# Optimization experiments

Measured on AMD Instinct MI355X. Metric: run time of the kernel, lower is better.

## Reference

```python
import jax, jax.numpy as jnp
import numpy as np

N = 50000      # nodes
E = 800000     # edges (before self-loops)
F_IN = 128     # num_features
H = 4          # heads
C = 64         # hidden_channels
HC = H * C     # 256
NEG_SLOPE = 0.2


def setup_inputs() -> dict:
    key = jax.random.key(0)
    ks = jax.random.split(key, 20)
    x = jax.random.normal(ks[0], (N, F_IN), dtype=jnp.float32)
    edge_index = jax.random.randint(ks[1], (2, E), 0, N, dtype=jnp.int32)
    s = 0.05
    inp = {"x": x, "edge_index": edge_index}
    dims_in = [F_IN, HC, HC, HC]
    for l in range(4):
        kW, ka, kb = jax.random.split(ks[2 + l], 3)
        inp[f"W{l+1}"] = jax.random.normal(kW, (dims_in[l], HC), dtype=jnp.float32) * s
        inp[f"a_src{l+1}"] = jax.random.normal(ka, (H, C), dtype=jnp.float32) * s
        inp[f"a_dst{l+1}"] = jax.random.normal(kb, (H, C), dtype=jnp.float32) * s
        inp[f"b{l+1}"] = jnp.zeros((HC,), dtype=jnp.float32)
    return inp


def gat_conv(x, src, dst, W, a_src, a_dst, b):
    # x: [N, F_in] -> h: [N, H, C]
    h = (x @ W).reshape(N, H, C)
    es = jnp.sum(h * a_src, axis=-1)  # [N, H] per-node source logits
    ed = jnp.sum(h * a_dst, axis=-1)  # [N, H]
    e = jax.nn.leaky_relu(es[src] + ed[dst], NEG_SLOPE)  # [Etot, H]
    m = jax.ops.segment_max(e, dst, num_segments=N)      # per-dst max
    m = jnp.where(jnp.isfinite(m), m, 0.0)
    ex = jnp.exp(e - m[dst])
    denom = jax.ops.segment_sum(ex, dst, num_segments=N)
    alpha = ex / (denom[dst] + 1e-16)                     # edge softmax
    out = jax.ops.segment_sum(alpha[:, :, None] * h[src], dst, num_segments=N)
    return out.reshape(N, HC) + b


def reference(x, edge_index,
              W1, a_src1, a_dst1, b1,
              W2, a_src2, a_dst2, b2,
              W3, a_src3, a_dst3, b3,
              W4, a_src4, a_dst4, b4):
    loop = jnp.arange(N, dtype=edge_index.dtype)
    src = jnp.concatenate([edge_index[0], loop])  # add self-loops (PyG default)
    dst = jnp.concatenate([edge_index[1], loop])
    x1 = jax.nn.relu(gat_conv(x, src, dst, W1, a_src1, a_dst1, b1))
    x2 = jax.nn.relu(gat_conv(x1, src, dst, W2, a_src2, a_dst2, b2))
    x3 = jax.nn.relu(gat_conv(x2 + x1, src, dst, W3, a_src3, a_dst3, b3))
    x4 = jax.nn.relu(gat_conv(x2 + x3, src, dst, W4, a_src4, a_dst4, b4))
    # NOTE: source code calls conv4 again (not conv5) -- reproduced faithfully
    x5 = gat_conv(x4 + x3, src, dst, W4, a_src4, a_dst4, b4)
    return x5
```

## Files before the change

### kernel.cpp

```cpp
#include <hip/hip_runtime.h>
#include <hip/hip_bf16.h>

#define N_NODES 50000
#define E_EDGES 800000
#define ETOT (E_EDGES + N_NODES)
#define HC 256
#define NHEAD 4
#define CHAN 64
#define NEG 0.2f
#define NBLK ((N_NODES + 1023) / 1024)

typedef _Float16 half8 __attribute__((ext_vector_type(8)));
typedef _Float16 half4v __attribute__((ext_vector_type(4)));
typedef float float4v __attribute__((ext_vector_type(4)));


__global__ void count_kernel(const int* __restrict__ ei, int* __restrict__ counts) {
    int i = blockIdx.x * blockDim.x + threadIdx.x;
    if (i >= ETOT) return;
    int dst = (i < E_EDGES) ? ei[E_EDGES + i] : (i - E_EDGES);
    atomicAdd(&counts[dst], 1);
}

__global__ __launch_bounds__(256) void blocksum_kernel(const int* __restrict__ counts,
                                                       int* __restrict__ blocksums) {
    __shared__ int s[4];
    int b = blockIdx.x, tid = threadIdx.x;
    int base = b * 1024;
    int sum = 0;
    #pragma unroll
    for (int r = 0; r < 4; ++r) {
        int idx = base + r * 256 + tid;
        sum += (idx < N_NODES) ? counts[idx] : 0;
    }
    #pragma unroll
    for (int m = 1; m < 64; m <<= 1) sum += __shfl_xor(sum, m, 64);
    if ((tid & 63) == 0) s[tid >> 6] = sum;
    __syncthreads();
    if (tid == 0) blocksums[b] = s[0] + s[1] + s[2] + s[3];
}

__global__ __launch_bounds__(64) void blockscan_kernel(int* __restrict__ blocksums) {
    int tid = threadIdx.x;
    int v = (tid < NBLK) ? blocksums[tid] : 0;
    #pragma unroll
    for (int off = 1; off < 64; off <<= 1) {
        int t = __shfl_up(v, off, 64);
        if (tid >= off) v += t;
    }
    if (tid < NBLK) blocksums[tid] = v;
}

__global__ __launch_bounds__(1024) void scatter_scan_kernel(const int* __restrict__ counts,
                                                            const int* __restrict__ blocksums,
                                                            int* __restrict__ offsets,
                                                            int* __restrict__ cursor) {
    __shared__ int s[1024];
    int b = blockIdx.x, tid = threadIdx.x;
    int idx = b * 1024 + tid;
    int v = (idx < N_NODES) ? counts[idx] : 0;
    s[tid] = v;
    __syncthreads();
    for (int off = 1; off < 1024; off <<= 1) {
        int t = (tid >= off) ? s[tid - off] : 0;
        __syncthreads();
        s[tid] += t;
        __syncthreads();
    }
    int excl = s[tid] - v + (b > 0 ? blocksums[b - 1] : 0);
    if (idx < N_NODES) { offsets[idx] = excl; cursor[idx] = excl; }
    if (idx == N_NODES - 1) offsets[N_NODES] = excl + v;
}

__global__ void fill_kernel(const int* __restrict__ ei, int* __restrict__ cursor,
                            int* __restrict__ csr_src) {
    int i = blockIdx.x * blockDim.x + threadIdx.x;
    if (i >= ETOT) return;
    int src, dst;
    if (i < E_EDGES) { src = ei[i]; dst = ei[E_EDGES + i]; }
    else             { src = i - E_EDGES; dst = src; }
    int pos = atomicAdd(&cursor[dst], 1);
    csr_src[pos] = src;
}


__global__ void wsplit_kernel(const float* __restrict__ W, _Float16* __restrict__ Wth,
                              _Float16* __restrict__ Wtl, int K) {
    int id = blockIdx.x * 256 + threadIdx.x;
    if (id >= K * 256) return;
    int n = id & 255, k = id >> 8;
    float w = W[(size_t)k * 256 + n];
    _Float16 h = (_Float16)w;
    _Float16 l = (_Float16)(w - (float)h);
    Wth[(size_t)n * K + k] = h;
    Wtl[(size_t)n * K + k] = l;
}

__global__ void xsplit_kernel(const float* __restrict__ x, _Float16* __restrict__ xh,
                              _Float16* __restrict__ xl, int total) {
    int id = blockIdx.x * 256 + threadIdx.x;
    if (id >= total) return;
    float v = x[id];
    _Float16 h = (_Float16)v;
    xh[id] = h;
    xl[id] = (_Float16)(v - (float)h);
}


#define LDK 40

__global__ __launch_bounds__(256) void gemm_mfma_kernel(
        const _Float16* __restrict__ A1h, const _Float16* __restrict__ A1l,
        const _Float16* __restrict__ A2h,
        const _Float16* __restrict__ Wth, const _Float16* __restrict__ Wtl,
        const float* __restrict__ a_src, const float* __restrict__ a_dst,
        _Float16* __restrict__ H16, float* __restrict__ es, float* __restrict__ ed,
        int M, int K) {
    __shared__ _Float16 Ah[64][LDK];
    __shared__ _Float16 Al[64][LDK];
    __shared__ _Float16 Bh[256][LDK];
    __shared__ _Float16 Bl[256][LDK];

    int tid = threadIdx.x;
    int m0 = blockIdx.x * 64;
    int w = tid >> 6, lane = tid & 63;
    int rn = w * 64;
    int fr = lane & 15;
    int q  = lane >> 4;
    int fk = q * 8;

    int wr = tid >> 2;
    int wk = (tid & 3) * 8;

    bool has_lo = (A1l != nullptr);
    bool has2   = (A2h != nullptr);

    float4v acc[4][4];
    #pragma unroll
    for (int i = 0; i < 4; ++i)
        #pragma unroll
        for (int j = 0; j < 4; ++j)
            acc[i][j] = (float4v){0.f, 0.f, 0.f, 0.f};

    half8 pa, pal, pbh[4], pbl[4];

    auto load_tile = [&](int k0) {
        int row = m0 + wr;
        pa  = (half8)(_Float16)0;
        pal = (half8)(_Float16)0;
        if (row < M) {
            pa = *(const half8*)(A1h + (size_t)row * K + k0 + wk);
            if (has2) {
                half8 u = *(const half8*)(A2h + (size_t)row * K + k0 + wk);
                pa = pa + u;
            }
            if (has_lo) pal = *(const half8*)(A1l + (size_t)row * K + k0 + wk);
        }
        #pragma unroll
        for (int g = 0; g < 4; ++g) {
            int r = g * 64 + wr;
            pbh[g] = *(const half8*)(Wth + (size_t)r * K + k0 + wk);
            pbl[g] = *(const half8*)(Wtl + (size_t)r * K + k0 + wk);
        }
    };

    load_tile(0);
    for (int k0 = 0; k0 < K; k0 += 32) {
        *(half8*)&Ah[wr][wk] = pa;
        if (has_lo) *(half8*)&Al[wr][wk] = pal;
        #pragma unroll
        for (int g = 0; g < 4; ++g) {
            int r = g * 64 + wr;
            *(half8*)&Bh[r][wk] = pbh[g];
            *(half8*)&Bl[r][wk] = pbl[g];
        }
        __syncthreads();
        if (k0 + 32 < K) load_tile(k0 + 32);
        half8 afh[4], bfh[4], bfl[4];
        #pragma unroll
        for (int t = 0; t < 4; ++t) {
            afh[t] = *(const half8*)&Ah[t * 16 + fr][fk];
            bfh[t] = *(const half8*)&Bh[rn + t * 16 + fr][fk];
            bfl[t] = *(const half8*)&Bl[rn + t * 16 + fr][fk];
        }
        if (has_lo) {
            half8 afl[4];
            #pragma unroll
            for (int t = 0; t < 4; ++t) afl[t] = *(const half8*)&Al[t * 16 + fr][fk];
            #pragma unroll
            for (int tm = 0; tm < 4; ++tm)
                #pragma unroll
                for (int tn = 0; tn < 4; ++tn)
                    acc[tm][tn] = __builtin_amdgcn_mfma_f32_16x16x32_f16(
                        afl[tm], bfh[tn], acc[tm][tn], 0, 0, 0);
        }
        #pragma unroll
        for (int tm = 0; tm < 4; ++tm)
            #pragma unroll
            for (int tn = 0; tn < 4; ++tn) {
                float4v c = acc[tm][tn];
                c = __builtin_amdgcn_mfma_f32_16x16x32_f16(afh[tm], bfl[tn], c, 0, 0, 0);
                c = __builtin_amdgcn_mfma_f32_16x16x32_f16(afh[tm], bfh[tn], c, 0, 0, 0);
                acc[tm][tn] = c;
            }
        __syncthreads();
    }

    float asv[4], adv[4];
    #pragma unroll
    for (int tn = 0; tn < 4; ++tn) {
        asv[tn] = a_src[w * CHAN + tn * 16 + fr];
        adv[tn] = a_dst[w * CHAN + tn * 16 + fr];
    }
    #pragma unroll
    for (int tm = 0; tm < 4; ++tm) {
        #pragma unroll
        for (int i = 0; i < 4; ++i) {
            int row = m0 + tm * 16 + q * 4 + i;
            float ps = 0.f, pd = 0.f;
            #pragma unroll
            for (int tn = 0; tn < 4; ++tn) {
                float hv = acc[tm][tn][i];
                ps += hv * asv[tn];
                pd += hv * adv[tn];
                if (row < M)
                    H16[(size_t)row * HC + rn + tn * 16 + fr] = (_Float16)hv;
            }
            #pragma unroll
            for (int msk = 1; msk < 16; msk <<= 1) {
                ps += __shfl_xor(ps, msk, 64);
                pd += __shfl_xor(pd, msk, 64);
            }
            if (fr == 0 && row < M) {
                es[row * NHEAD + w] = ps;
                ed[row * NHEAD + w] = pd;
            }
        }
    }
}


__global__ __launch_bounds__(256) void gat_aggregate_kernel(
        const _Float16* __restrict__ H16, const float* __restrict__ es, const float* __restrict__ ed,
        const int* __restrict__ offsets, const int* __restrict__ csr_src,
        const float* __restrict__ bias, _Float16* __restrict__ out16,
        float* __restrict__ out32, int do_relu) {
    __shared__ float ex_lds[4][256];
    __shared__ int   src_lds[4][64];
    int tid = threadIdx.x;
    int w = tid >> 6, lane = tid & 63;
    int n = blockIdx.x * 4 + w;
    int off = offsets[n];
    int deg = offsets[n + 1] - off;
    float4 edv = *(const float4*)(ed + (size_t)n * 4);

    if (deg <= 64) {
        int sreg = n;
        float4 ex4 = make_float4(0.f, 0.f, 0.f, 0.f);
        if (lane < deg) {
            sreg = csr_src[off + lane];
            float4 esv = *(const float4*)(es + (size_t)sreg * 4);
            float4 e4;
            e4.x = esv.x + edv.x; e4.y = esv.y + edv.y;
            e4.z = esv.z + edv.z; e4.w = esv.w + edv.w;
            e4.x = (e4.x > 0.f) ? e4.x : NEG * e4.x;
            e4.y = (e4.y > 0.f) ? e4.y : NEG * e4.y;
            e4.z = (e4.z > 0.f) ? e4.z : NEG * e4.z;
            e4.w = (e4.w > 0.f) ? e4.w : NEG * e4.w;
            ex4.x = __expf(e4.x); ex4.y = __expf(e4.y);
            ex4.z = __expf(e4.z); ex4.w = __expf(e4.w);
        }
        src_lds[w][lane] = sreg;
        *(float4*)&ex_lds[w][lane * 4] = ex4;

        int hl = lane & 31, side = lane >> 5;
        int hd = hl >> 3;
        float av[8] = {0.f, 0.f, 0.f, 0.f, 0.f, 0.f, 0.f, 0.f};
        int degr = (deg + 7) & ~7;
        #pragma unroll 2
        for (int j0 = 0; j0 < degr; j0 += 8) {
            int j = j0 + side;
            int s0 = src_lds[w][j];
            int s1 = src_lds[w][j + 2];
            int s2 = src_lds[w][j + 4];
            int s3 = src_lds[w][j + 6];
            float w0 = ex_lds[w][j * 4 + hd];
            float w1 = ex_lds[w][(j + 2) * 4 + hd];
            float w2 = ex_lds[w][(j + 4) * 4 + hd];
            float w3 = ex_lds[w][(j + 6) * 4 + hd];
            half8 h0 = *(const half8*)(H16 + (size_t)s0 * HC + hl * 8);
            half8 h1 = *(const half8*)(H16 + (size_t)s1 * HC + hl * 8);
            half8 h2 = *(const half8*)(H16 + (size_t)s2 * HC + hl * 8);
            half8 h3 = *(const half8*)(H16 + (size_t)s3 * HC + hl * 8);
            #pragma unroll
            for (int c = 0; c < 8; ++c) {
                av[c] += w0 * (float)h0[c];
                av[c] += w1 * (float)h1[c];
                av[c] += w2 * (float)h2[c];
                av[c] += w3 * (float)h3[c];
            }
        }

        float4 l4 = ex4;
        #pragma unroll
        for (int msk = 1; msk < 64; msk <<= 1) {
            l4.x += __shfl_xor(l4.x, msk, 64);
            l4.y += __shfl_xor(l4.y, msk, 64);
            l4.z += __shfl_xor(l4.z, msk, 64);
            l4.w += __shfl_xor(l4.w, msk, 64);
        }
        #pragma unroll
        for (int c = 0; c < 8; ++c) av[c] += __shfl_xor(av[c], 32, 64);
        if (side == 0) {
            float denom = (hd == 0) ? l4.x : (hd == 1) ? l4.y : (hd == 2) ? l4.z : l4.w;
            float scale = 1.f / (denom + 1e-16f);
            float4 b0 = *(const float4*)(bias + hl * 8);
            float4 b1 = *(const float4*)(bias + hl * 8 + 4);
            float o[8] = {av[0] * scale + b0.x, av[1] * scale + b0.y,
                          av[2] * scale + b0.z, av[3] * scale + b0.w,
                          av[4] * scale + b1.x, av[5] * scale + b1.y,
                          av[6] * scale + b1.z, av[7] * scale + b1.w};
            if (do_relu)
                #pragma unroll
                for (int c = 0; c < 8; ++c) o[c] = fmaxf(o[c], 0.f);
            if (out16) {
                half8 ov = {(_Float16)o[0], (_Float16)o[1], (_Float16)o[2], (_Float16)o[3],
                            (_Float16)o[4], (_Float16)o[5], (_Float16)o[6], (_Float16)o[7]};
                *(half8*)(out16 + (size_t)n * HC + hl * 8) = ov;
            } else {
                *(float4*)(out32 + (size_t)n * HC + hl * 8) =
                    make_float4(o[0], o[1], o[2], o[3]);
                *(float4*)(out32 + (size_t)n * HC + hl * 8 + 4) =
                    make_float4(o[4], o[5], o[6], o[7]);
            }
        }
        return;
    }

    int head = lane >> 4;
    float4 acc0 = make_float4(0.f, 0.f, 0.f, 0.f);
    float m[4] = {-1e30f, -1e30f, -1e30f, -1e30f};
    float l[4] = {0.f, 0.f, 0.f, 0.f};
    for (int base = 0; base < deg; base += 64) {
        int j = base + lane;
        if (j < deg) {
            int s = csr_src[off + j];
            float4 esv = *(const float4*)(es + (size_t)s * 4);
            float e[4] = {esv.x + edv.x, esv.y + edv.y, esv.z + edv.z, esv.w + edv.w};
            #pragma unroll
            for (int h = 0; h < 4; ++h) {
                e[h] = (e[h] > 0.f) ? e[h] : NEG * e[h];
                float M2 = fmaxf(m[h], e[h]);
                l[h] = l[h] * __expf(m[h] - M2) + __expf(e[h] - M2);
                m[h] = M2;
            }
        }
    }
    #pragma unroll
    for (int msk = 1; msk < 64; msk <<= 1) {
        #pragma unroll
        for (int h = 0; h < 4; ++h) {
            float mo = __shfl_xor(m[h], msk, 64);
            float lo = __shfl_xor(l[h], msk, 64);
            float M2 = fmaxf(m[h], mo);
            l[h] = l[h] * __expf(m[h] - M2) + lo * __expf(mo - M2);
            m[h] = M2;
        }
    }
    float fm = m[head];
    float fr2 = 1.f / (l[head] + 1e-16f);
    float edh = ((const float*)&edv)[head];
    for (int j = 0; j < deg; ++j) {
        int s = csr_src[off + j];
        float e = es[(size_t)s * 4 + head] + edh;
        e = (e > 0.f) ? e : NEG * e;
        float alpha = __expf(e - fm) * fr2;
        half4v h0 = *(const half4v*)(H16 + (size_t)s * HC + lane * 4);
        acc0.x += alpha * (float)h0[0]; acc0.y += alpha * (float)h0[1];
        acc0.z += alpha * (float)h0[2]; acc0.w += alpha * (float)h0[3];
    }
    float4 b4 = *(const float4*)(bias + lane * 4);
    float o[4] = {acc0.x + b4.x, acc0.y + b4.y, acc0.z + b4.z, acc0.w + b4.w};
    if (do_relu)
        #pragma unroll
        for (int c = 0; c < 4; ++c) o[c] = fmaxf(o[c], 0.f);
    if (out16) {
        half4v ov = {(_Float16)o[0], (_Float16)o[1], (_Float16)o[2], (_Float16)o[3]};
        *(half4v*)(out16 + (size_t)n * HC + lane * 4) = ov;
    } else {
        *(float4*)(out32 + (size_t)n * HC + lane * 4) = make_float4(o[0], o[1], o[2], o[3]);
    }
}


extern "C" void kernel_launch(void* const* d_in, const int* in_sizes, int n_in,
                              void* d_out, int out_size, void* d_ws, size_t ws_size,
                              hipStream_t stream) {
    const float* x  = (const float*)d_in[0];
    const int*   ei = (const int*)d_in[1];
    const float *W[5], *Asrc[5], *Adst[5], *Bs[5];
    for (int l = 0; l < 4; ++l) {
        W[l]    = (const float*)d_in[2 + l * 4];
        Asrc[l] = (const float*)d_in[3 + l * 4];
        Adst[l] = (const float*)d_in[4 + l * 4];
        Bs[l]   = (const float*)d_in[5 + l * 4];
    }
    W[4] = W[3]; Asrc[4] = Asrc[3]; Adst[4] = Adst[3]; Bs[4] = Bs[3];

    char* ws = (char*)d_ws;
    size_t off = 0;
    auto alloc = [&](size_t bytes) -> void* {
        void* p = ws + off;
        off += (bytes + 255) & ~(size_t)255;
        return p;
    };
    _Float16* h16  = (_Float16*)alloc((size_t)N_NODES * HC * 2);
    _Float16* xa   = (_Float16*)alloc((size_t)N_NODES * HC * 2);
    _Float16* xb   = (_Float16*)alloc((size_t)N_NODES * HC * 2);
    _Float16* xc   = (_Float16*)alloc((size_t)N_NODES * HC * 2);
    _Float16* xd   = (_Float16*)alloc((size_t)N_NODES * HC * 2);
    _Float16* xh   = (_Float16*)alloc((size_t)N_NODES * 128 * 2);
    _Float16* xl   = (_Float16*)alloc((size_t)N_NODES * 128 * 2);
    float* es      = (float*)alloc((size_t)N_NODES * 4 * 4);
    float* ed      = (float*)alloc((size_t)N_NODES * 4 * 4);
    int*   counts  = (int*)alloc((size_t)N_NODES * 4);
    int*   offsets = (int*)alloc((size_t)(N_NODES + 1) * 4);
    int*   cursor  = (int*)alloc((size_t)N_NODES * 4);
    int*   csr_src = (int*)alloc((size_t)ETOT * 4);
    int*   blocksums = (int*)alloc((size_t)NBLK * 4);
    _Float16 *Wth[5], *Wtl[5];
    int Ks[4] = {128, 256, 256, 256};
    for (int l = 0; l < 4; ++l) {
        Wth[l] = (_Float16*)alloc((size_t)256 * Ks[l] * 2);
        Wtl[l] = (_Float16*)alloc((size_t)256 * Ks[l] * 2);
    }
    Wth[4] = Wth[3]; Wtl[4] = Wtl[3];

    hipMemsetAsync(counts, 0, (size_t)N_NODES * 4, stream);
    count_kernel<<<(ETOT + 255) / 256, 256, 0, stream>>>(ei, counts);
    blocksum_kernel<<<NBLK, 256, 0, stream>>>(counts, blocksums);
    blockscan_kernel<<<1, 64, 0, stream>>>(blocksums);
    scatter_scan_kernel<<<NBLK, 1024, 0, stream>>>(counts, blocksums, offsets, cursor);
    fill_kernel<<<(ETOT + 255) / 256, 256, 0, stream>>>(ei, cursor, csr_src);
    for (int l = 0; l < 4; ++l)
        wsplit_kernel<<<(Ks[l] * 256 + 255) / 256, 256, 0, stream>>>(W[l], Wth[l], Wtl[l], Ks[l]);
    xsplit_kernel<<<(N_NODES * 128 + 255) / 256, 256, 0, stream>>>(x, xh, xl, N_NODES * 128);

    auto layer = [&](const _Float16* a1h, const _Float16* a1l, const _Float16* a2h,
                     int K, int l, _Float16* o16, float* o32, int relu) {
        gemm_mfma_kernel<<<(N_NODES + 63) / 64, 256, 0, stream>>>(
            a1h, a1l, a2h, Wth[l], Wtl[l], Asrc[l], Adst[l], h16, es, ed, N_NODES, K);
        gat_aggregate_kernel<<<N_NODES / 4, 256, 0, stream>>>(
            h16, es, ed, offsets, csr_src, Bs[l], o16, o32, relu);
    };

    float* out = (float*)d_out;
    layer(xh, xl,      nullptr, 128, 0, xa, nullptr, 1);
    layer(xa, nullptr, nullptr, 256, 1, xb, nullptr, 1);
    layer(xb, nullptr, xa,      256, 2, xc, nullptr, 1);
    layer(xb, nullptr, xc,      256, 3, xd, nullptr, 1);
    layer(xd, nullptr, xc,      256, 4, nullptr, out, 0);
}
```

Before: 792.2 us.

## Precompute per-edge attention exponentials in separate edge-parallel kernel

```diff
diff --git a/kernel.cpp b/kernel.cpp
--- a/kernel.cpp
+++ b/kernel.cpp
@@ -73,7 +73,7 @@
 }
 
 __global__ void fill_kernel(const int* __restrict__ ei, int* __restrict__ cursor,
-                            int* __restrict__ csr_src) {
+                            int* __restrict__ csr_src, int* __restrict__ csr_dst) {
     int i = blockIdx.x * blockDim.x + threadIdx.x;
     if (i >= ETOT) return;
     int src, dst;
@@ -81,6 +81,7 @@
     else             { src = i - E_EDGES; dst = src; }
     int pos = atomicAdd(&cursor[dst], 1);
     csr_src[pos] = src;
+    csr_dst[pos] = dst;
 }
 
 
@@ -104,6 +105,28 @@
     _Float16 h = (_Float16)v;
     xh[id] = h;
     xl[id] = (_Float16)(v - (float)h);
+}
+
+
+__global__ __launch_bounds__(256) void edge_alpha_kernel(
+        const float* __restrict__ es, const float* __restrict__ ed,
+        const int* __restrict__ csr_src, const int* __restrict__ csr_dst,
+        float* __restrict__ ex) {
+    int e = blockIdx.x * 256 + threadIdx.x;
+    if (e >= ETOT) return;
+    int s = csr_src[e], d = csr_dst[e];
+    float4 esv = *(const float4*)(es + (size_t)s * 4);
+    float4 edv = *(const float4*)(ed + (size_t)d * 4);
+    float4 v;
+    v.x = esv.x + edv.x; v.y = esv.y + edv.y;
+    v.z = esv.z + edv.z; v.w = esv.w + edv.w;
+    v.x = (v.x > 0.f) ? v.x : NEG * v.x;
+    v.y = (v.y > 0.f) ? v.y : NEG * v.y;
+    v.z = (v.z > 0.f) ? v.z : NEG * v.z;
+    v.w = (v.w > 0.f) ? v.w : NEG * v.w;
+    v.x = __expf(v.x); v.y = __expf(v.y);
+    v.z = __expf(v.z); v.w = __expf(v.w);
+    *(float4*)(ex + (size_t)e * 4) = v;
 }
 
 
@@ -241,7 +264,7 @@
 
 
 __global__ __launch_bounds__(256) void gat_aggregate_kernel(
-        const _Float16* __restrict__ H16, const float* __restrict__ es, const float* __restrict__ ed,
+        const _Float16* __restrict__ H16, const float* __restrict__ ex,
         const int* __restrict__ offsets, const int* __restrict__ csr_src,
         const float* __restrict__ bias, _Float16* __restrict__ out16,
         float* __restrict__ out32, int do_relu) {
@@ -252,23 +275,13 @@
     int n = blockIdx.x * 4 + w;
     int off = offsets[n];
     int deg = offsets[n + 1] - off;
-    float4 edv = *(const float4*)(ed + (size_t)n * 4);
 
     if (deg <= 64) {
         int sreg = n;
         float4 ex4 = make_float4(0.f, 0.f, 0.f, 0.f);
         if (lane < deg) {
             sreg = csr_src[off + lane];
-            float4 esv = *(const float4*)(es + (size_t)sreg * 4);
-            float4 e4;
-            e4.x = esv.x + edv.x; e4.y = esv.y + edv.y;
-            e4.z = esv.z + edv.z; e4.w = esv.w + edv.w;
-            e4.x = (e4.x > 0.f) ? e4.x : NEG * e4.x;
-            e4.y = (e4.y > 0.f) ? e4.y : NEG * e4.y;
-            e4.z = (e4.z > 0.f) ? e4.z : NEG * e4.z;
-            e4.w = (e4.w > 0.f) ? e4.w : NEG * e4.w;
-            ex4.x = __expf(e4.x); ex4.y = __expf(e4.y);
-            ex4.z = __expf(e4.z); ex4.w = __expf(e4.w);
+            ex4 = *(const float4*)(ex + (size_t)(off + lane) * 4);
         }
         src_lds[w][lane] = sreg;
         *(float4*)&ex_lds[w][lane * 4] = ex4;
@@ -339,48 +352,19 @@
 
     int head = lane >> 4;
     float4 acc0 = make_float4(0.f, 0.f, 0.f, 0.f);
-    float m[4] = {-1e30f, -1e30f, -1e30f, -1e30f};
-    float l[4] = {0.f, 0.f, 0.f, 0.f};
-    for (int base = 0; base < deg; base += 64) {
-        int j = base + lane;
-        if (j < deg) {
-            int s = csr_src[off + j];
-            float4 esv = *(const float4*)(es + (size_t)s * 4);
-            float e[4] = {esv.x + edv.x, esv.y + edv.y, esv.z + edv.z, esv.w + edv.w};
-            #pragma unroll
-            for (int h = 0; h < 4; ++h) {
-                e[h] = (e[h] > 0.f) ? e[h] : NEG * e[h];
-                float M2 = fmaxf(m[h], e[h]);
-                l[h] = l[h] * __expf(m[h] - M2) + __expf(e[h] - M2);
-                m[h] = M2;
-            }
-        }
-    }
-    #pragma unroll
-    for (int msk = 1; msk < 64; msk <<= 1) {
-        #pragma unroll
-        for (int h = 0; h < 4; ++h) {
-            float mo = __shfl_xor(m[h], msk, 64);
-            float lo = __shfl_xor(l[h], msk, 64);
-            float M2 = fmaxf(m[h], mo);
-            l[h] = l[h] * __expf(m[h] - M2) + lo * __expf(mo - M2);
-            m[h] = M2;
-        }
-    }
-    float fm = m[head];
-    float fr2 = 1.f / (l[head] + 1e-16f);
-    float edh = ((const float*)&edv)[head];
+    float den = 0.f;
     for (int j = 0; j < deg; ++j) {
         int s = csr_src[off + j];
-        float e = es[(size_t)s * 4 + head] + edh;
-        e = (e > 0.f) ? e : NEG * e;
-        float alpha = __expf(e - fm) * fr2;
+        float exv = ex[(size_t)(off + j) * 4 + head];
+        den += exv;
         half4v h0 = *(const half4v*)(H16 + (size_t)s * HC + lane * 4);
-        acc0.x += alpha * (float)h0[0]; acc0.y += alpha * (float)h0[1];
-        acc0.z += alpha * (float)h0[2]; acc0.w += alpha * (float)h0[3];
-    }
+        acc0.x += exv * (float)h0[0]; acc0.y += exv * (float)h0[1];
+        acc0.z += exv * (float)h0[2]; acc0.w += exv * (float)h0[3];
+    }
+    float scale = 1.f / (den + 1e-16f);
     float4 b4 = *(const float4*)(bias + lane * 4);
-    float o[4] = {acc0.x + b4.x, acc0.y + b4.y, acc0.z + b4.z, acc0.w + b4.w};
+    float o[4] = {acc0.x * scale + b4.x, acc0.y * scale + b4.y,
+                  acc0.z * scale + b4.z, acc0.w * scale + b4.w};
     if (do_relu)
         #pragma unroll
         for (int c = 0; c < 4; ++c) o[c] = fmaxf(o[c], 0.f);
@@ -423,10 +407,12 @@
     _Float16* xl   = (_Float16*)alloc((size_t)N_NODES * 128 * 2);
     float* es      = (float*)alloc((size_t)N_NODES * 4 * 4);
     float* ed      = (float*)alloc((size_t)N_NODES * 4 * 4);
+    float* exbuf   = (float*)alloc((size_t)ETOT * 4 * 4);
     int*   counts  = (int*)alloc((size_t)N_NODES * 4);
     int*   offsets = (int*)alloc((size_t)(N_NODES + 1) * 4);
     int*   cursor  = (int*)alloc((size_t)N_NODES * 4);
     int*   csr_src = (int*)alloc((size_t)ETOT * 4);
+    int*   csr_dst = (int*)alloc((size_t)ETOT * 4);
     int*   blocksums = (int*)alloc((size_t)NBLK * 4);
     _Float16 *Wth[5], *Wtl[5];
     int Ks[4] = {128, 256, 256, 256};
@@ -441,7 +427,7 @@
     blocksum_kernel<<<NBLK, 256, 0, stream>>>(counts, blocksums);
     blockscan_kernel<<<1, 64, 0, stream>>>(blocksums);
     scatter_scan_kernel<<<NBLK, 1024, 0, stream>>>(counts, blocksums, offsets, cursor);
-    fill_kernel<<<(ETOT + 255) / 256, 256, 0, stream>>>(ei, cursor, csr_src);
+    fill_kernel<<<(ETOT + 255) / 256, 256, 0, stream>>>(ei, cursor, csr_src, csr_dst);
     for (int l = 0; l < 4; ++l)
         wsplit_kernel<<<(Ks[l] * 256 + 255) / 256, 256, 0, stream>>>(W[l], Wth[l], Wtl[l], Ks[l]);
     xsplit_kernel<<<(N_NODES * 128 + 255) / 256, 256, 0, stream>>>(x, xh, xl, N_NODES * 128);
@@ -450,8 +436,10 @@
                      int K, int l, _Float16* o16, float* o32, int relu) {
         gemm_mfma_kernel<<<(N_NODES + 63) / 64, 256, 0, stream>>>(
             a1h, a1l, a2h, Wth[l], Wtl[l], Asrc[l], Adst[l], h16, es, ed, N_NODES, K);
+        edge_alpha_kernel<<<(ETOT + 255) / 256, 256, 0, stream>>>(
+            es, ed, csr_src, csr_dst, exbuf);
         gat_aggregate_kernel<<<N_NODES / 4, 256, 0, stream>>>(
-            h16, es, ed, offsets, csr_src, Bs[l], o16, o32, relu);
+            h16, exbuf, offsets, csr_src, Bs[l], o16, o32, relu);
     };
 
     float* out = (float*)d_out;
```

New measurement: 749.2 us. -5.4%, faster.
